# Optimization experiments

Hardware: AMD Instinct MI355X
Metric: run time of the kernel (lower is better)

Reference implementation:

```python
import jax, jax.numpy as jnp
import numpy as np

NEG_SLOPE = 0.2  # LeakyReLU slope used by GAT attention
EPS = 1e-16


def gat_conv(x, edge_index, W, a_src, a_dst, b):
    """One GATConv layer with 'mean' head aggregation.
    x: [N, Fin], edge_index: [2, E] (row 0 = src/j, row 1 = dst/i),
    W: [Fin, H*F], a_src/a_dst: [H, F], b: [F].
    Returns [N, F].
    """
    N = x.shape[0]
    H, F = a_src.shape
    h = (x @ W).reshape(N, H, F)                      # [N, H, F]
    src, dst = edge_index[0], edge_index[1]
    # per-node attention halves, gathered per edge
    as_ = jnp.einsum('nhf,hf->nh', h, a_src)          # [N, H]
    ad_ = jnp.einsum('nhf,hf->nh', h, a_dst)          # [N, H]
    e = jax.nn.leaky_relu(as_[src] + ad_[dst], NEG_SLOPE)  # [E, H]
    # segment softmax over incoming edges of each dst node
    m = jax.ops.segment_max(e, dst, num_segments=N)   # [N, H]
    ex = jnp.exp(e - m[dst])                          # [E, H]
    denom = jax.ops.segment_sum(ex, dst, num_segments=N)
    alpha = ex / (denom[dst] + EPS)                   # [E, H]
    # weighted scatter-aggregate of source features
    out = jax.ops.segment_sum(alpha[:, :, None] * h[src], dst, num_segments=N)  # [N, H, F]
    return out.mean(axis=1) + b                       # mean over heads


def setup_inputs() -> dict:
    key = jax.random.key(0)
    ks = jax.random.split(key, 10)
    N, E = 100000, 1000000
    in_dim, hid, out_dim, H = 128, 32, 16, 4
    x = jax.random.normal(ks[0], (N, in_dim), dtype=jnp.float32)
    edge_index = jax.random.randint(ks[1], (2, E), 0, N, dtype=jnp.int64)
    s1 = 1.0 / np.sqrt(in_dim)
    s2 = 1.0 / np.sqrt(hid)
    W1 = jax.random.uniform(ks[2], (in_dim, H * hid), jnp.float32, -s1, s1)
    a1_src = jax.random.uniform(ks[3], (H, hid), jnp.float32, -s2, s2)
    a1_dst = jax.random.uniform(ks[4], (H, hid), jnp.float32, -s2, s2)
    b1 = jnp.zeros((hid,), jnp.float32)
    s3 = 1.0 / np.sqrt(out_dim)
    W2 = jax.random.uniform(ks[5], (hid, H * out_dim), jnp.float32, -s2, s2)
    a2_src = jax.random.uniform(ks[6], (H, out_dim), jnp.float32, -s3, s3)
    a2_dst = jax.random.uniform(ks[7], (H, out_dim), jnp.float32, -s3, s3)
    b2 = jnp.zeros((out_dim,), jnp.float32)
    return {"x": x, "edge_index": edge_index,
            "W1": W1, "a1_src": a1_src, "a1_dst": a1_dst, "b1": b1,
            "W2": W2, "a2_src": a2_src, "a2_dst": a2_dst, "b2": b2}


def reference(x, edge_index, W1, a1_src, a1_dst, b1, W2, a2_src, a2_dst, b2):
    h = gat_conv(x, edge_index, W1, a1_src, a1_dst, b1)
    h = jax.nn.relu(h)
    # dropout is identity in eval mode
    out = gat_conv(h, edge_index, W2, a2_src, a2_dst, b2)
    return out
```

## Files before the change

kernel.cpp:

```cpp
#include <hip/hip_runtime.h>
#include <math.h>

#define NEG_SLOPE 0.2f
#define EPS_GAT 1e-16f
#define LOG2E 1.4426950408889634f
typedef unsigned int u32;
typedef unsigned short u16;
typedef __attribute__((ext_vector_type(8))) short short8;
typedef __attribute__((ext_vector_type(4))) float f32x4;

__device__ inline u16 f2bf(float x) {
    union { float f; u32 u; } v; v.f = x;
    u32 r = v.u + 0x7FFFu + ((v.u >> 16) & 1u);
    return (u16)(r >> 16);
}
__device__ inline float bf_lo(u32 u) {
    union { u32 i; float f; } v; v.i = u << 16; return v.f;
}
__device__ inline float bf_hi(u32 u) {
    union { u32 i; float f; } v; v.i = u & 0xFFFF0000u; return v.f;
}
__device__ inline float bf1(u16 s) {
    union { u32 i; float f; } v; v.i = ((u32)s) << 16; return v.f;
}
__device__ inline float fast_exp2(float x) {
#if __has_builtin(__builtin_amdgcn_exp2f)
    return __builtin_amdgcn_exp2f(x);
#else
    return exp2f(x);
#endif
}
__device__ inline float lrelu_exp2(float t) {
    return fast_exp2(fmaxf(t, NEG_SLOPE * t));
}


__global__ void degree_prep_kernel(const int* __restrict__ dst, int E,
                                   int* __restrict__ counts, int* __restrict__ rank,
                                   const float* __restrict__ W1,
                                   u16* __restrict__ w1t_hi, u16* __restrict__ w1t_lo,
                                   const float* __restrict__ W2, const float* __restrict__ a2s,
                                   const float* __restrict__ a2d, float* __restrict__ w_as,
                                   float* __restrict__ w_ad, int degBlocks) {
    int b = blockIdx.x;
    if (b < degBlocks) {
        int e = b * 256 + threadIdx.x;
        if (e < E) rank[e] = atomicAdd(&counts[dst[e]], 1);
    } else if (b < degBlocks + 64) {
        int i = (b - degBlocks) * 256 + threadIdx.x;
        int k = i >> 7, n = i & 127;
        float w = W1[i];
        u16 hi = f2bf(w);
        u16 lo = f2bf(w - bf1(hi));
        w1t_hi[n * 128 + k] = hi;
        w1t_lo[n * 128 + k] = lo;
    } else {
        int t = threadIdx.x;
        if (t < 128) {
            int h = t >> 5, k = t & 31;
            float s1 = 0.f, s2 = 0.f;
#pragma unroll
            for (int f = 0; f < 16; ++f) {
                float w = W2[k * 64 + h * 16 + f];
                s1 += w * a2s[h * 16 + f];
                s2 += w * a2d[h * 16 + f];
            }
            w_as[h * 32 + k] = s1;
            w_ad[h * 32 + k] = s2;
        }
    }
}

__global__ __launch_bounds__(1024) void scan_block_kernel(const int* __restrict__ counts, int N,
                                                          int* __restrict__ scanned, int* __restrict__ bsums) {
    __shared__ int tmp[1024];
    int i = blockIdx.x * 1024 + threadIdx.x;
    int v = (i < N) ? counts[i] : 0;
    tmp[threadIdx.x] = v;
    __syncthreads();
    for (int d = 1; d < 1024; d <<= 1) {
        int t = (threadIdx.x >= d) ? tmp[threadIdx.x - d] : 0;
        __syncthreads();
        tmp[threadIdx.x] += t;
        __syncthreads();
    }
    if (i < N) scanned[i] = tmp[threadIdx.x];
    if (threadIdx.x == 1023) bsums[blockIdx.x] = tmp[1023];
}

__global__ __launch_bounds__(256) void scan_partials_kernel(int* __restrict__ bsums, int nb) {
    __shared__ int tmp[256];
    int tid = threadIdx.x;
    int v = (tid < nb) ? bsums[tid] : 0;
    tmp[tid] = v;
    __syncthreads();
    for (int d = 1; d < 256; d <<= 1) {
        int t = (tid >= d) ? tmp[tid - d] : 0;
        __syncthreads();
        tmp[tid] += t;
        __syncthreads();
    }
    if (tid < nb) bsums[tid] = tmp[tid] - v;
}

__global__ void finalize_offsets_kernel(const int* __restrict__ scanned,
                                        const int* __restrict__ bsums_excl, int N,
                                        int* __restrict__ row_off) {
    int i = blockIdx.x * blockDim.x + threadIdx.x;
    if (i < N) {
        int incl = scanned[i] + bsums_excl[i >> 10];
        row_off[i + 1] = incl;
        if (i == 0) row_off[0] = 0;
    }
}

__global__ void fill_csr_kernel(const int* __restrict__ src, const int* __restrict__ dst, int E,
                                const int* __restrict__ row_off, const int* __restrict__ rank,
                                int* __restrict__ csr_src) {
    int e = blockIdx.x * blockDim.x + threadIdx.x;
    if (e < E) {
        int pos = row_off[dst[e]] + rank[e];
        csr_src[pos] = src[e];
    }
}


__global__ __launch_bounds__(256) void gemm1_mfma_kernel(const float* __restrict__ X,
                                                         const u16* __restrict__ w1t_hi,
                                                         const u16* __restrict__ w1t_lo,
                                                         const float* __restrict__ a_src,
                                                         const float* __restrict__ a_dst,
                                                         u16* __restrict__ Hb,
                                                         float* __restrict__ as_,
                                                         float* __restrict__ ad_, int N) {
    __shared__ u16 xsh_hi[64][40];
    __shared__ u16 xsh_lo[64][40];
    __shared__ u16 wbuf[10240];
    __shared__ float ash[128], adsh[128];
    u16* wsh_hi = wbuf;
    u16* wsh_lo = wbuf + 5120;
    int tid = threadIdx.x;
    int wave = tid >> 6, lane = tid & 63, quad = lane >> 4;
    int m0 = blockIdx.x * 64;

    if (tid < 128) { ash[tid] = a_src[tid]; adsh[tid] = a_dst[tid]; }

    f32x4 acc[4][2];
#pragma unroll
    for (int rt = 0; rt < 4; ++rt)
#pragma unroll
        for (int ct = 0; ct < 2; ++ct) acc[rt][ct] = (f32x4)(0.f);

    int xrow = tid >> 2, xkq = (tid & 3) * 8;

    for (int k0 = 0; k0 < 128; k0 += 32) {
        {
            int gr = m0 + xrow;
            float f[8];
            *(float4*)&f[0] = (gr < N) ? *(const float4*)(X + (size_t)gr * 128 + k0 + xkq)
                                       : make_float4(0.f, 0.f, 0.f, 0.f);
            *(float4*)&f[4] = (gr < N) ? *(const float4*)(X + (size_t)gr * 128 + k0 + xkq + 4)
                                       : make_float4(0.f, 0.f, 0.f, 0.f);
            u16 hi[8], lo[8];
#pragma unroll
            for (int i = 0; i < 8; ++i) {
                hi[i] = f2bf(f[i]);
                lo[i] = f2bf(f[i] - bf1(hi[i]));
            }
            *(uint4*)&xsh_hi[xrow][xkq] = *(uint4*)hi;
            *(uint4*)&xsh_lo[xrow][xkq] = *(uint4*)lo;
        }
        {
#pragma unroll
            for (int i = 0; i < 2; ++i) {
                int id = tid * 2 + i;
                int n = id >> 2, part = id & 3;
                *(uint4*)&wsh_hi[n * 40 + part * 8] =
                    ((const uint4*)(w1t_hi + n * 128 + k0))[part];
                *(uint4*)&wsh_lo[n * 40 + part * 8] =
                    ((const uint4*)(w1t_lo + n * 128 + k0))[part];
            }
        }
        __syncthreads();

        short8 bhi[2], blo[2];
#pragma unroll
        for (int ct = 0; ct < 2; ++ct) {
            int n = wave * 32 + ct * 16 + (lane & 15);
            bhi[ct] = *(const short8*)&wsh_hi[n * 40 + quad * 8];
            blo[ct] = *(const short8*)&wsh_lo[n * 40 + quad * 8];
        }
#pragma unroll
        for (int rt = 0; rt < 4; ++rt) {
            int m = rt * 16 + (lane & 15);
            short8 ahi = *(const short8*)&xsh_hi[m][quad * 8];
            short8 alo = *(const short8*)&xsh_lo[m][quad * 8];
#pragma unroll
            for (int ct = 0; ct < 2; ++ct) {
                acc[rt][ct] = __builtin_amdgcn_mfma_f32_16x16x32_bf16(ahi, bhi[ct], acc[rt][ct], 0, 0, 0);
                acc[rt][ct] = __builtin_amdgcn_mfma_f32_16x16x32_bf16(alo, bhi[ct], acc[rt][ct], 0, 0, 0);
                acc[rt][ct] = __builtin_amdgcn_mfma_f32_16x16x32_bf16(ahi, blo[ct], acc[rt][ct], 0, 0, 0);
            }
        }
        __syncthreads();
    }

    const int HS = 130;
#pragma unroll
    for (int rt = 0; rt < 4; ++rt)
#pragma unroll
        for (int ct = 0; ct < 2; ++ct) {
            int col = wave * 32 + ct * 16 + (lane & 15);
#pragma unroll
            for (int r = 0; r < 4; ++r) {
                int row = rt * 16 + quad * 4 + r;
                u16 hv = f2bf(acc[rt][ct][r]);
                int gr = m0 + row;
                if (gr < N) Hb[(size_t)gr * 128 + col] = hv;
                wbuf[row * HS + col] = hv;
            }
        }
    __syncthreads();

    {
        int row = tid >> 2, h = tid & 3;
        int gr = m0 + row;
        if (gr < N) {
            const u32* hr = (const u32*)&wbuf[row * HS + h * 32];
            float s1 = 0.f, s2 = 0.f;
#pragma unroll
            for (int q = 0; q < 16; ++q) {
                u32 u = hr[q];
                float flo = bf_lo(u), fhi = bf_hi(u);
                s1 += flo * ash[h * 32 + 2 * q] + fhi * ash[h * 32 + 2 * q + 1];
                s2 += flo * adsh[h * 32 + 2 * q] + fhi * adsh[h * 32 + 2 * q + 1];
            }
            as_[(size_t)gr * 4 + h] = s1 * LOG2E;
            ad_[(size_t)gr * 4 + h] = s2 * LOG2E;
        }
    }
}


__global__ __launch_bounds__(256) void node_agg128_kernel(const u32* __restrict__ Hb,
                                                          const float* __restrict__ as_,
                                                          const float* __restrict__ ad_,
                                                          const int* __restrict__ row_off,
                                                          const int* __restrict__ csr_src,
                                                          const float* __restrict__ bias,
                                                          const float* __restrict__ w_as,
                                                          const float* __restrict__ w_ad,
                                                          u32* __restrict__ O1,
                                                          float* __restrict__ as2,
                                                          float* __restrict__ ad2, int N) {
    int lane = threadIdx.x & 63;
    int node = __builtin_amdgcn_readfirstlane(blockIdx.x * 4 + (threadIdx.x >> 6));
    if (node >= N) return;
    int start = __builtin_amdgcn_readfirstlane(row_off[node]);
    int end   = __builtin_amdgcn_readfirstlane(row_off[node + 1]);
    int deg = end - start;
    int h = lane >> 4;
    float adh = ad_[node * 4 + h];

    int clamp = (deg > 0) ? deg - 1 : 0;
    int vidx = csr_src[start + min(lane, clamp)];
    int m = min(deg, 64);

    float2 acc = make_float2(0.f, 0.f);
    float den = 0.f;
    int j = 0;
    for (; j + 4 <= m; j += 4) {
        int s0 = __builtin_amdgcn_readlane(vidx, j);
        int s1 = __builtin_amdgcn_readlane(vidx, j + 1);
        int s2 = __builtin_amdgcn_readlane(vidx, j + 2);
        int s3 = __builtin_amdgcn_readlane(vidx, j + 3);
        float a0 = as_[s0 * 4 + h], a1 = as_[s1 * 4 + h];
        float a2 = as_[s2 * 4 + h], a3 = as_[s3 * 4 + h];
        u32 u0 = Hb[s0 * 64 + lane];
        u32 u1 = Hb[s1 * 64 + lane];
        u32 u2 = Hb[s2 * 64 + lane];
        u32 u3 = Hb[s3 * 64 + lane];
        float e0 = lrelu_exp2(a0 + adh), e1 = lrelu_exp2(a1 + adh);
        float e2 = lrelu_exp2(a2 + adh), e3 = lrelu_exp2(a3 + adh);
        acc.x = fmaf(e0, bf_lo(u0), acc.x); acc.y = fmaf(e0, bf_hi(u0), acc.y); den += e0;
        acc.x = fmaf(e1, bf_lo(u1), acc.x); acc.y = fmaf(e1, bf_hi(u1), acc.y); den += e1;
        acc.x = fmaf(e2, bf_lo(u2), acc.x); acc.y = fmaf(e2, bf_hi(u2), acc.y); den += e2;
        acc.x = fmaf(e3, bf_lo(u3), acc.x); acc.y = fmaf(e3, bf_hi(u3), acc.y); den += e3;
    }
    for (; j < m; ++j) {
        int s = __builtin_amdgcn_readlane(vidx, j);
        float e = lrelu_exp2(as_[s * 4 + h] + adh);
        u32 u = Hb[s * 64 + lane];
        acc.x = fmaf(e, bf_lo(u), acc.x); acc.y = fmaf(e, bf_hi(u), acc.y); den += e;
    }
    for (int jj = start + 64; jj < end; ++jj) {
        int s = __builtin_amdgcn_readfirstlane(csr_src[jj]);
        float e = lrelu_exp2(as_[s * 4 + h] + adh);
        u32 u = Hb[s * 64 + lane];
        acc.x = fmaf(e, bf_lo(u), acc.x); acc.y = fmaf(e, bf_hi(u), acc.y); den += e;
    }
    float inv = 1.f / (den + EPS_GAT);
    float px = acc.x * inv, py = acc.y * inv;
    px += __shfl_xor(px, 16); py += __shfl_xor(py, 16);
    px += __shfl_xor(px, 32); py += __shfl_xor(py, 32);

    int f2 = (lane & 15) * 2;
    float2 bv = *(const float2*)&bias[f2];
    float ox = fmaxf(px * 0.25f + bv.x, 0.f);
    float oy = fmaxf(py * 0.25f + bv.y, 0.f);
    if (lane < 16)
        O1[node * 16 + lane] = (u32)f2bf(ox) | ((u32)f2bf(oy) << 16);

    int h2 = lane >> 4;
    float2 wa = *(const float2*)&w_as[h2 * 32 + f2];
    float2 wd = *(const float2*)&w_ad[h2 * 32 + f2];
    float ta = ox * wa.x + oy * wa.y;
    float td = ox * wd.x + oy * wd.y;
    ta += __shfl_xor(ta, 1); td += __shfl_xor(td, 1);
    ta += __shfl_xor(ta, 2); td += __shfl_xor(td, 2);
    ta += __shfl_xor(ta, 4); td += __shfl_xor(td, 4);
    ta += __shfl_xor(ta, 8); td += __shfl_xor(td, 8);
    if ((lane & 15) == 0) {
        as2[node * 4 + h2] = ta * LOG2E;
        ad2[node * 4 + h2] = td * LOG2E;
    }
}


__global__ __launch_bounds__(256) void node_agg32_fused_kernel(const u32* __restrict__ O1,
                                                               const float* __restrict__ as_,
                                                               const float* __restrict__ ad_,
                                                               const int* __restrict__ row_off,
                                                               const int* __restrict__ csr_src,
                                                               const float* __restrict__ W2,
                                                               const float* __restrict__ b2,
                                                               float* __restrict__ Out, int N) {
    __shared__ float w2sh[2048];
    __shared__ float aggsh[4][136];
    int tid = threadIdx.x;
    {
        float4 v = ((const float4*)W2)[tid];
        *(float4*)&w2sh[tid * 4] = v;
        float4 v2 = ((const float4*)W2)[tid + 256];
        *(float4*)&w2sh[(tid + 256) * 4] = v2;
    }

    int lane = tid & 63;
    int nb = tid >> 6;
    int node = __builtin_amdgcn_readfirstlane(blockIdx.x * 4 + nb);
    bool active = node < N;
    int h = lane >> 4, f = lane & 15;
    if (active) {
        int start = __builtin_amdgcn_readfirstlane(row_off[node]);
        int end   = __builtin_amdgcn_readfirstlane(row_off[node + 1]);
        int deg = end - start;
        float adh = ad_[node * 4 + h];

        int clamp = (deg > 0) ? deg - 1 : 0;
        int vidx = csr_src[start + min(lane, clamp)];
        int m = min(deg, 64);

        float2 acc = make_float2(0.f, 0.f);
        float den = 0.f;
        int j = 0;
        for (; j + 4 <= m; j += 4) {
            int s0 = __builtin_amdgcn_readlane(vidx, j);
            int s1 = __builtin_amdgcn_readlane(vidx, j + 1);
            int s2 = __builtin_amdgcn_readlane(vidx, j + 2);
            int s3 = __builtin_amdgcn_readlane(vidx, j + 3);
            float a0 = as_[s0 * 4 + h], a1 = as_[s1 * 4 + h];
            float a2 = as_[s2 * 4 + h], a3 = as_[s3 * 4 + h];
            u32 u0 = O1[s0 * 16 + f];
            u32 u1 = O1[s1 * 16 + f];
            u32 u2 = O1[s2 * 16 + f];
            u32 u3 = O1[s3 * 16 + f];
            float e0 = lrelu_exp2(a0 + adh), e1 = lrelu_exp2(a1 + adh);
            float e2 = lrelu_exp2(a2 + adh), e3 = lrelu_exp2(a3 + adh);
            acc.x = fmaf(e0, bf_lo(u0), acc.x); acc.y = fmaf(e0, bf_hi(u0), acc.y); den += e0;
            acc.x = fmaf(e1, bf_lo(u1), acc.x); acc.y = fmaf(e1, bf_hi(u1), acc.y); den += e1;
            acc.x = fmaf(e2, bf_lo(u2), acc.x); acc.y = fmaf(e2, bf_hi(u2), acc.y); den += e2;
            acc.x = fmaf(e3, bf_lo(u3), acc.x); acc.y = fmaf(e3, bf_hi(u3), acc.y); den += e3;
        }
        for (; j < m; ++j) {
            int s = __builtin_amdgcn_readlane(vidx, j);
            float e = lrelu_exp2(as_[s * 4 + h] + adh);
            u32 u = O1[s * 16 + f];
            acc.x = fmaf(e, bf_lo(u), acc.x); acc.y = fmaf(e, bf_hi(u), acc.y); den += e;
        }
        for (int jj = start + 64; jj < end; ++jj) {
            int s = __builtin_amdgcn_readfirstlane(csr_src[jj]);
            float e = lrelu_exp2(as_[s * 4 + h] + adh);
            u32 u = O1[s * 16 + f];
            acc.x = fmaf(e, bf_lo(u), acc.x); acc.y = fmaf(e, bf_hi(u), acc.y); den += e;
        }
        float inv = 1.f / (den + EPS_GAT);
        aggsh[nb][h * 34 + f * 2]     = acc.x * inv;
        aggsh[nb][h * 34 + f * 2 + 1] = acc.y * inv;
    }
    __syncthreads();

    if (active) {
        int q = h, o = f;
        float s = 0.f;
#pragma unroll
        for (int k = 0; k < 32; ++k)
            s += aggsh[nb][q * 34 + k] * w2sh[k * 64 + q * 16 + o];
        s += __shfl_xor(s, 16);
        s += __shfl_xor(s, 32);
        if (lane < 16)
            Out[(size_t)node * 16 + o] = s * 0.25f + b2[o];
    }
}


extern "C" void kernel_launch(void* const* d_in, const int* in_sizes, int n_in,
                              void* d_out, int out_size, void* d_ws, size_t ws_size,
                              hipStream_t stream) {
    const float* x      = (const float*)d_in[0];
    const int*   eidx   = (const int*)d_in[1];
    const float* W1     = (const float*)d_in[2];
    const float* a1_src = (const float*)d_in[3];
    const float* a1_dst = (const float*)d_in[4];
    const float* b1     = (const float*)d_in[5];
    const float* W2     = (const float*)d_in[6];
    const float* a2_src = (const float*)d_in[7];
    const float* a2_dst = (const float*)d_in[8];
    const float* b2     = (const float*)d_in[9];
    float* out = (float*)d_out;

    const int N = in_sizes[0] / 128;
    const int E = in_sizes[1] / 2;
    const int* src = eidx;
    const int* dst = eidx + E;

    char* base = (char*)d_ws;
    size_t off = 0;
    auto carve = [&](size_t bytes) -> char* {
        off = (off + 255) & ~(size_t)255;
        char* p = base + off;
        off += bytes;
        return p;
    };
    int* counts   = (int*)carve((size_t)N * 4);
    int* scanned  = (int*)carve((size_t)N * 4);
    int* bsums    = (int*)carve(256 * 4);
    int* row_off  = (int*)carve((size_t)(N + 1) * 4);
    int* rank     = (int*)carve((size_t)E * 4);
    int* csr_src  = (int*)carve((size_t)E * 4);
    u16* w1t_hi   = (u16*)carve(128 * 128 * 2);
    u16* w1t_lo   = (u16*)carve(128 * 128 * 2);
    u16* h1b      = (u16*)carve((size_t)N * 128 * 2);
    u32* out1b    = (u32*)carve((size_t)N * 16 * 4);
    float* as1  = (float*)carve((size_t)N * 4 * 4);
    float* ad1  = (float*)carve((size_t)N * 4 * 4);
    float* as2  = (float*)carve((size_t)N * 4 * 4);
    float* ad2  = (float*)carve((size_t)N * 4 * 4);
    float* w_as = (float*)carve(4 * 32 * 4);
    float* w_ad = (float*)carve(4 * 32 * 4);
    (void)ws_size; (void)n_in; (void)out_size;

    hipMemsetAsync(counts, 0, (size_t)N * 4, stream);
    int degBlocks = (E + 255) / 256;
    degree_prep_kernel<<<degBlocks + 65, 256, 0, stream>>>(dst, E, counts, rank,
                                                           W1, w1t_hi, w1t_lo,
                                                           W2, a2_src, a2_dst, w_as, w_ad,
                                                           degBlocks);
    int nb = (N + 1023) / 1024;
    scan_block_kernel<<<nb, 1024, 0, stream>>>(counts, N, scanned, bsums);
    scan_partials_kernel<<<1, 256, 0, stream>>>(bsums, nb);
    finalize_offsets_kernel<<<(N + 255) / 256, 256, 0, stream>>>(scanned, bsums, N, row_off);
    fill_csr_kernel<<<(E + 255) / 256, 256, 0, stream>>>(src, dst, E, row_off, rank, csr_src);

    gemm1_mfma_kernel<<<(N + 63) / 64, 256, 0, stream>>>(x, w1t_hi, w1t_lo, a1_src, a1_dst,
                                                         h1b, as1, ad1, N);
    node_agg128_kernel<<<(N + 3) / 4, 256, 0, stream>>>((const u32*)h1b, as1, ad1,
                                                        row_off, csr_src, b1, w_as, w_ad,
                                                        out1b, as2, ad2, N);

    node_agg32_fused_kernel<<<(N + 3) / 4, 256, 0, stream>>>(out1b, as2, ad2, row_off,
                                                             csr_src, W2, b2, out, N);
}
```

Baseline: 298.5 us.

## Merge CSR build and layer-1 GEMM into one cooperative persistent kernel

Replaces the memset, degree count, three scan kernels, CSR fill and the GEMM1 launch with a single cooperative kernel that separates phases with grid-wide syncs. Within one phase, part of the grid runs the GEMM tiles while the remaining blocks do the degree atomics, so the two overlap. This removes several launch gaps and small-kernel tails, at the cost of grid.sync overhead, a fixed persistent grid size, and fewer blocks per phase.

```diff
diff --git a/kernel.cpp b/kernel.cpp
--- a/kernel.cpp
+++ b/kernel.cpp
@@ -1,5 +1,8 @@
 #include <hip/hip_runtime.h>
+#include <hip/hip_cooperative_groups.h>
 #include <math.h>
+
+namespace cg = cooperative_groups;
 
 #define NEG_SLOPE 0.2f
 #define EPS_GAT 1e-16f
@@ -35,209 +38,222 @@
 }
 
 
-__global__ void degree_prep_kernel(const int* __restrict__ dst, int E,
-                                   int* __restrict__ counts, int* __restrict__ rank,
-                                   const float* __restrict__ W1,
-                                   u16* __restrict__ w1t_hi, u16* __restrict__ w1t_lo,
-                                   const float* __restrict__ W2, const float* __restrict__ a2s,
-                                   const float* __restrict__ a2d, float* __restrict__ w_as,
-                                   float* __restrict__ w_ad, int degBlocks) {
-    int b = blockIdx.x;
-    if (b < degBlocks) {
-        int e = b * 256 + threadIdx.x;
-        if (e < E) rank[e] = atomicAdd(&counts[dst[e]], 1);
-    } else if (b < degBlocks + 64) {
-        int i = (b - degBlocks) * 256 + threadIdx.x;
+struct CoopArgs {
+    const int* src; const int* dst; int E; int N;
+    int* counts; int* rank;
+    const float* X; const float* W1;
+    const float* a1_src; const float* a1_dst;
+    const float* W2; const float* a2s; const float* a2d;
+    float* w_as; float* w_ad;
+    u16* w1t_hi; u16* w1t_lo;
+    u16* Hb; float* as1; float* ad1;
+    int* scanned; int* bsums; int* row_off; int* csr_src;
+    int gemmBlocks;
+};
+
+__global__ __launch_bounds__(256) void coop_kernel(CoopArgs A) {
+    cg::grid_group grid = cg::this_grid();
+    __shared__ __align__(16) u16 xsh_hi[64 * 40];
+    __shared__ __align__(16) u16 xsh_lo[64 * 40];
+    __shared__ __align__(16) u16 wbuf[10240];
+    __shared__ float ash[128], adsh[128];
+    int* stmp = (int*)xsh_hi;
+
+    int tid = threadIdx.x, bid = blockIdx.x;
+    int nB = gridDim.x;
+    int gtid = bid * 256 + tid, gstride = nB * 256;
+
+    for (int i = gtid; i < A.N; i += gstride) A.counts[i] = 0;
+    for (int i = gtid; i < 16384; i += gstride) {
         int k = i >> 7, n = i & 127;
-        float w = W1[i];
+        float w = A.W1[i];
         u16 hi = f2bf(w);
         u16 lo = f2bf(w - bf1(hi));
-        w1t_hi[n * 128 + k] = hi;
-        w1t_lo[n * 128 + k] = lo;
+        A.w1t_hi[n * 128 + k] = hi;
+        A.w1t_lo[n * 128 + k] = lo;
+    }
+    if (gtid < 128) {
+        int h = gtid >> 5, k = gtid & 31;
+        float s1 = 0.f, s2 = 0.f;
+#pragma unroll
+        for (int f = 0; f < 16; ++f) {
+            float w = A.W2[k * 64 + h * 16 + f];
+            s1 += w * A.a2s[h * 16 + f];
+            s2 += w * A.a2d[h * 16 + f];
+        }
+        A.w_as[h * 32 + k] = s1;
+        A.w_ad[h * 32 + k] = s2;
+    }
+    grid.sync();
+
+    if (bid < A.gemmBlocks) {
+        if (tid < 128) { ash[tid] = A.a1_src[tid]; adsh[tid] = A.a1_dst[tid]; }
+        u16* wsh_hi = wbuf;
+        u16* wsh_lo = wbuf + 5120;
+        int wave = tid >> 6, lane = tid & 63, quad = lane >> 4;
+        int xrow = tid >> 2, xkq = (tid & 3) * 8;
+        int tiles = (A.N + 63) >> 6;
+        for (int t = bid; t < tiles; t += A.gemmBlocks) {
+            __syncthreads();
+            int m0 = t * 64;
+            f32x4 acc[4][2];
+#pragma unroll
+            for (int rt = 0; rt < 4; ++rt)
+#pragma unroll
+                for (int ct = 0; ct < 2; ++ct) acc[rt][ct] = (f32x4)(0.f);
+
+            for (int k0 = 0; k0 < 128; k0 += 32) {
+                {
+                    int gr = m0 + xrow;
+                    float f[8];
+                    *(float4*)&f[0] = (gr < A.N) ? *(const float4*)(A.X + (size_t)gr * 128 + k0 + xkq)
+                                                 : make_float4(0.f, 0.f, 0.f, 0.f);
+                    *(float4*)&f[4] = (gr < A.N) ? *(const float4*)(A.X + (size_t)gr * 128 + k0 + xkq + 4)
+                                                 : make_float4(0.f, 0.f, 0.f, 0.f);
+                    u16 hi[8], lo[8];
+#pragma unroll
+                    for (int i = 0; i < 8; ++i) {
+                        hi[i] = f2bf(f[i]);
+                        lo[i] = f2bf(f[i] - bf1(hi[i]));
+                    }
+                    *(uint4*)&xsh_hi[xrow * 40 + xkq] = *(uint4*)hi;
+                    *(uint4*)&xsh_lo[xrow * 40 + xkq] = *(uint4*)lo;
+                }
+                {
+#pragma unroll
+                    for (int i = 0; i < 2; ++i) {
+                        int id = tid * 2 + i;
+                        int n = id >> 2, part = id & 3;
+                        *(uint4*)&wsh_hi[n * 40 + part * 8] =
+                            ((const uint4*)(A.w1t_hi + n * 128 + k0))[part];
+                        *(uint4*)&wsh_lo[n * 40 + part * 8] =
+                            ((const uint4*)(A.w1t_lo + n * 128 + k0))[part];
+                    }
+                }
+                __syncthreads();
+
+                short8 bhi[2], blo[2];
+#pragma unroll
+                for (int ct = 0; ct < 2; ++ct) {
+                    int n = wave * 32 + ct * 16 + (lane & 15);
+                    bhi[ct] = *(const short8*)&wsh_hi[n * 40 + quad * 8];
+                    blo[ct] = *(const short8*)&wsh_lo[n * 40 + quad * 8];
+                }
+#pragma unroll
+                for (int rt = 0; rt < 4; ++rt) {
+                    int m = rt * 16 + (lane & 15);
+                    short8 ahi = *(const short8*)&xsh_hi[m * 40 + quad * 8];
+                    short8 alo = *(const short8*)&xsh_lo[m * 40 + quad * 8];
+#pragma unroll
+                    for (int ct = 0; ct < 2; ++ct) {
+                        acc[rt][ct] = __builtin_amdgcn_mfma_f32_16x16x32_bf16(ahi, bhi[ct], acc[rt][ct], 0, 0, 0);
+                        acc[rt][ct] = __builtin_amdgcn_mfma_f32_16x16x32_bf16(alo, bhi[ct], acc[rt][ct], 0, 0, 0);
+                        acc[rt][ct] = __builtin_amdgcn_mfma_f32_16x16x32_bf16(ahi, blo[ct], acc[rt][ct], 0, 0, 0);
+                    }
+                }
+                __syncthreads();
+            }
+
+            const int HS = 130;
+#pragma unroll
+            for (int rt = 0; rt < 4; ++rt)
+#pragma unroll
+                for (int ct = 0; ct < 2; ++ct) {
+                    int col = wave * 32 + ct * 16 + (lane & 15);
+#pragma unroll
+                    for (int r = 0; r < 4; ++r) {
+                        int row = rt * 16 + quad * 4 + r;
+                        u16 hv = f2bf(acc[rt][ct][r]);
+                        int gr = m0 + row;
+                        if (gr < A.N) A.Hb[(size_t)gr * 128 + col] = hv;
+                        wbuf[row * HS + col] = hv;
+                    }
+                }
+            __syncthreads();
+
+            {
+                int row = tid >> 2, h = tid & 3;
+                int gr = m0 + row;
+                if (gr < A.N) {
+                    const u32* hr = (const u32*)&wbuf[row * HS + h * 32];
+                    float s1 = 0.f, s2 = 0.f;
+#pragma unroll
+                    for (int q = 0; q < 16; ++q) {
+                        u32 u = hr[q];
+                        float flo = bf_lo(u), fhi = bf_hi(u);
+                        s1 += flo * ash[h * 32 + 2 * q] + fhi * ash[h * 32 + 2 * q + 1];
+                        s2 += flo * adsh[h * 32 + 2 * q] + fhi * adsh[h * 32 + 2 * q + 1];
+                    }
+                    A.as1[(size_t)gr * 4 + h] = s1 * LOG2E;
+                    A.ad1[(size_t)gr * 4 + h] = s2 * LOG2E;
+                }
+            }
+        }
     } else {
-        int t = threadIdx.x;
-        if (t < 128) {
-            int h = t >> 5, k = t & 31;
-            float s1 = 0.f, s2 = 0.f;
-#pragma unroll
-            for (int f = 0; f < 16; ++f) {
-                float w = W2[k * 64 + h * 16 + f];
-                s1 += w * a2s[h * 16 + f];
-                s2 += w * a2d[h * 16 + f];
+        int nd = nB - A.gemmBlocks;
+        for (int e = (bid - A.gemmBlocks) * 256 + tid; e < A.E; e += nd * 256)
+            A.rank[e] = atomicAdd(&A.counts[A.dst[e]], 1);
+    }
+    grid.sync();
+
+    {
+        int chunks = (A.N + 1023) >> 10;
+        for (int c = bid; c < chunks; c += nB) {
+            int idx = (c << 10) + tid * 4;
+            int4 v = make_int4(0, 0, 0, 0);
+            if (idx + 3 < A.N) v = *(const int4*)(A.counts + idx);
+            else {
+                if (idx < A.N)     v.x = A.counts[idx];
+                if (idx + 1 < A.N) v.y = A.counts[idx + 1];
+                if (idx + 2 < A.N) v.z = A.counts[idx + 2];
             }
-            w_as[h * 32 + k] = s1;
-            w_ad[h * 32 + k] = s2;
-        }
-    }
-}
-
-__global__ __launch_bounds__(1024) void scan_block_kernel(const int* __restrict__ counts, int N,
-                                                          int* __restrict__ scanned, int* __restrict__ bsums) {
-    __shared__ int tmp[1024];
-    int i = blockIdx.x * 1024 + threadIdx.x;
-    int v = (i < N) ? counts[i] : 0;
-    tmp[threadIdx.x] = v;
-    __syncthreads();
-    for (int d = 1; d < 1024; d <<= 1) {
-        int t = (threadIdx.x >= d) ? tmp[threadIdx.x - d] : 0;
+            int p0 = v.x, p1 = p0 + v.y, p2 = p1 + v.z, p3 = p2 + v.w;
+            __syncthreads();
+            stmp[tid] = p3;
+            __syncthreads();
+            for (int d = 1; d < 256; d <<= 1) {
+                int t_ = (tid >= d) ? stmp[tid - d] : 0;
+                __syncthreads();
+                stmp[tid] += t_;
+                __syncthreads();
+            }
+            int excl = stmp[tid] - p3;
+            if (idx + 3 < A.N) {
+                int4 o = make_int4(excl + p0, excl + p1, excl + p2, excl + p3);
+                *(int4*)(A.scanned + idx) = o;
+            } else {
+                if (idx < A.N)     A.scanned[idx]     = excl + p0;
+                if (idx + 1 < A.N) A.scanned[idx + 1] = excl + p1;
+                if (idx + 2 < A.N) A.scanned[idx + 2] = excl + p2;
+            }
+            if (tid == 255) A.bsums[c] = stmp[255];
+        }
+    }
+    grid.sync();
+
+    if (bid == 0) {
+        int chunks = (A.N + 1023) >> 10;
+        int v = (tid < chunks) ? A.bsums[tid] : 0;
+        stmp[tid] = v;
         __syncthreads();
-        tmp[threadIdx.x] += t;
-        __syncthreads();
-    }
-    if (i < N) scanned[i] = tmp[threadIdx.x];
-    if (threadIdx.x == 1023) bsums[blockIdx.x] = tmp[1023];
-}
-
-__global__ __launch_bounds__(256) void scan_partials_kernel(int* __restrict__ bsums, int nb) {
-    __shared__ int tmp[256];
-    int tid = threadIdx.x;
-    int v = (tid < nb) ? bsums[tid] : 0;
-    tmp[tid] = v;
-    __syncthreads();
-    for (int d = 1; d < 256; d <<= 1) {
-        int t = (tid >= d) ? tmp[tid - d] : 0;
-        __syncthreads();
-        tmp[tid] += t;
-        __syncthreads();
-    }
-    if (tid < nb) bsums[tid] = tmp[tid] - v;
-}
-
-__global__ void finalize_offsets_kernel(const int* __restrict__ scanned,
-                                        const int* __restrict__ bsums_excl, int N,
-                                        int* __restrict__ row_off) {
-    int i = blockIdx.x * blockDim.x + threadIdx.x;
-    if (i < N) {
-        int incl = scanned[i] + bsums_excl[i >> 10];
-        row_off[i + 1] = incl;
-        if (i == 0) row_off[0] = 0;
-    }
-}
-
-__global__ void fill_csr_kernel(const int* __restrict__ src, const int* __restrict__ dst, int E,
-                                const int* __restrict__ row_off, const int* __restrict__ rank,
-                                int* __restrict__ csr_src) {
-    int e = blockIdx.x * blockDim.x + threadIdx.x;
-    if (e < E) {
-        int pos = row_off[dst[e]] + rank[e];
-        csr_src[pos] = src[e];
-    }
-}
-
-
-__global__ __launch_bounds__(256) void gemm1_mfma_kernel(const float* __restrict__ X,
-                                                         const u16* __restrict__ w1t_hi,
-                                                         const u16* __restrict__ w1t_lo,
-                                                         const float* __restrict__ a_src,
-                                                         const float* __restrict__ a_dst,
-                                                         u16* __restrict__ Hb,
-                                                         float* __restrict__ as_,
-                                                         float* __restrict__ ad_, int N) {
-    __shared__ u16 xsh_hi[64][40];
-    __shared__ u16 xsh_lo[64][40];
-    __shared__ u16 wbuf[10240];
-    __shared__ float ash[128], adsh[128];
-    u16* wsh_hi = wbuf;
-    u16* wsh_lo = wbuf + 5120;
-    int tid = threadIdx.x;
-    int wave = tid >> 6, lane = tid & 63, quad = lane >> 4;
-    int m0 = blockIdx.x * 64;
-
-    if (tid < 128) { ash[tid] = a_src[tid]; adsh[tid] = a_dst[tid]; }
-
-    f32x4 acc[4][2];
-#pragma unroll
-    for (int rt = 0; rt < 4; ++rt)
-#pragma unroll
-        for (int ct = 0; ct < 2; ++ct) acc[rt][ct] = (f32x4)(0.f);
-
-    int xrow = tid >> 2, xkq = (tid & 3) * 8;
-
-    for (int k0 = 0; k0 < 128; k0 += 32) {
-        {
-            int gr = m0 + xrow;
-            float f[8];
-            *(float4*)&f[0] = (gr < N) ? *(const float4*)(X + (size_t)gr * 128 + k0 + xkq)
-                                       : make_float4(0.f, 0.f, 0.f, 0.f);
-            *(float4*)&f[4] = (gr < N) ? *(const float4*)(X + (size_t)gr * 128 + k0 + xkq + 4)
-                                       : make_float4(0.f, 0.f, 0.f, 0.f);
-            u16 hi[8], lo[8];
-#pragma unroll
-            for (int i = 0; i < 8; ++i) {
-                hi[i] = f2bf(f[i]);
-                lo[i] = f2bf(f[i] - bf1(hi[i]));
-            }
-            *(uint4*)&xsh_hi[xrow][xkq] = *(uint4*)hi;
-            *(uint4*)&xsh_lo[xrow][xkq] = *(uint4*)lo;
-        }
-        {
-#pragma unroll
-            for (int i = 0; i < 2; ++i) {
-                int id = tid * 2 + i;
-                int n = id >> 2, part = id & 3;
-                *(uint4*)&wsh_hi[n * 40 + part * 8] =
-                    ((const uint4*)(w1t_hi + n * 128 + k0))[part];
-                *(uint4*)&wsh_lo[n * 40 + part * 8] =
-                    ((const uint4*)(w1t_lo + n * 128 + k0))[part];
-            }
-        }
-        __syncthreads();
-
-        short8 bhi[2], blo[2];
-#pragma unroll
-        for (int ct = 0; ct < 2; ++ct) {
-            int n = wave * 32 + ct * 16 + (lane & 15);
-            bhi[ct] = *(const short8*)&wsh_hi[n * 40 + quad * 8];
-            blo[ct] = *(const short8*)&wsh_lo[n * 40 + quad * 8];
-        }
-#pragma unroll
-        for (int rt = 0; rt < 4; ++rt) {
-            int m = rt * 16 + (lane & 15);
-            short8 ahi = *(const short8*)&xsh_hi[m][quad * 8];
-            short8 alo = *(const short8*)&xsh_lo[m][quad * 8];
-#pragma unroll
-            for (int ct = 0; ct < 2; ++ct) {
-                acc[rt][ct] = __builtin_amdgcn_mfma_f32_16x16x32_bf16(ahi, bhi[ct], acc[rt][ct], 0, 0, 0);
-                acc[rt][ct] = __builtin_amdgcn_mfma_f32_16x16x32_bf16(alo, bhi[ct], acc[rt][ct], 0, 0, 0);
-                acc[rt][ct] = __builtin_amdgcn_mfma_f32_16x16x32_bf16(ahi, blo[ct], acc[rt][ct], 0, 0, 0);
-            }
-        }
-        __syncthreads();
-    }
-
-    const int HS = 130;
-#pragma unroll
-    for (int rt = 0; rt < 4; ++rt)
-#pragma unroll
-        for (int ct = 0; ct < 2; ++ct) {
-            int col = wave * 32 + ct * 16 + (lane & 15);
-#pragma unroll
-            for (int r = 0; r < 4; ++r) {
-                int row = rt * 16 + quad * 4 + r;
-                u16 hv = f2bf(acc[rt][ct][r]);
-                int gr = m0 + row;
-                if (gr < N) Hb[(size_t)gr * 128 + col] = hv;
-                wbuf[row * HS + col] = hv;
-            }
-        }
-    __syncthreads();
-
-    {
-        int row = tid >> 2, h = tid & 3;
-        int gr = m0 + row;
-        if (gr < N) {
-            const u32* hr = (const u32*)&wbuf[row * HS + h * 32];
-            float s1 = 0.f, s2 = 0.f;
-#pragma unroll
-            for (int q = 0; q < 16; ++q) {
-                u32 u = hr[q];
-                float flo = bf_lo(u), fhi = bf_hi(u);
-                s1 += flo * ash[h * 32 + 2 * q] + fhi * ash[h * 32 + 2 * q + 1];
-                s2 += flo * adsh[h * 32 + 2 * q] + fhi * adsh[h * 32 + 2 * q + 1];
-            }
-            as_[(size_t)gr * 4 + h] = s1 * LOG2E;
-            ad_[(size_t)gr * 4 + h] = s2 * LOG2E;
-        }
+        for (int d = 1; d < 256; d <<= 1) {
+            int t_ = (tid >= d) ? stmp[tid - d] : 0;
+            __syncthreads();
+            stmp[tid] += t_;
+            __syncthreads();
+        }
+        if (tid < chunks) A.bsums[tid] = stmp[tid] - v;
+    }
+    grid.sync();
+
+    for (int i = gtid; i < A.N; i += gstride)
+        A.row_off[i + 1] = A.scanned[i] + A.bsums[i >> 10];
+    if (gtid == 0) A.row_off[0] = 0;
+    grid.sync();
+
+    for (int e = gtid; e < A.E; e += gstride) {
+        int pos = A.row_off[A.dst[e]] + A.rank[e];
+        A.csr_src[pos] = A.src[e];
     }
 }
 
@@ -459,24 +475,34 @@
     float* w_ad = (float*)carve(4 * 32 * 4);
     (void)ws_size; (void)n_in; (void)out_size;
 
-    hipMemsetAsync(counts, 0, (size_t)N * 4, stream);
-    int degBlocks = (E + 255) / 256;
-    degree_prep_kernel<<<degBlocks + 65, 256, 0, stream>>>(dst, E, counts, rank,
-                                                           W1, w1t_hi, w1t_lo,
-                                                           W2, a2_src, a2_dst, w_as, w_ad,
-                                                           degBlocks);
-    int nb = (N + 1023) / 1024;
-    scan_block_kernel<<<nb, 1024, 0, stream>>>(counts, N, scanned, bsums);
-    scan_partials_kernel<<<1, 256, 0, stream>>>(bsums, nb);
-    finalize_offsets_kernel<<<(N + 255) / 256, 256, 0, stream>>>(scanned, bsums, N, row_off);
-    fill_csr_kernel<<<(E + 255) / 256, 256, 0, stream>>>(src, dst, E, row_off, rank, csr_src);
-
-    gemm1_mfma_kernel<<<(N + 63) / 64, 256, 0, stream>>>(x, w1t_hi, w1t_lo, a1_src, a1_dst,
-                                                         h1b, as1, ad1, N);
+    int blocksPerCU = 2;
+    if (hipOccupancyMaxActiveBlocksPerMultiprocessor(&blocksPerCU, coop_kernel, 256, 0) != hipSuccess)
+        blocksPerCU = 2;
+    if (blocksPerCU < 1) blocksPerCU = 1;
+    if (blocksPerCU > 4) blocksPerCU = 4;
+    int grid = 256 * blocksPerCU;
+
+    CoopArgs A;
+    A.src = src; A.dst = dst; A.E = E; A.N = N;
+    A.counts = counts; A.rank = rank;
+    A.X = x; A.W1 = W1;
+    A.a1_src = a1_src; A.a1_dst = a1_dst;
+    A.W2 = W2; A.a2s = a2_src; A.a2d = a2_dst;
+    A.w_as = w_as; A.w_ad = w_ad;
+    A.w1t_hi = w1t_hi; A.w1t_lo = w1t_lo;
+    A.Hb = h1b; A.as1 = as1; A.ad1 = ad1;
+    A.scanned = scanned; A.bsums = bsums; A.row_off = row_off; A.csr_src = csr_src;
+    A.gemmBlocks = (grid * 3) / 5;
+    if (A.gemmBlocks < 1) A.gemmBlocks = 1;
+    if (A.gemmBlocks > grid - 1) A.gemmBlocks = grid - 1;
+
+    void* params[] = { &A };
+    hipLaunchCooperativeKernel((const void*)coop_kernel, dim3(grid), dim3(256),
+                               params, 0, stream);
+
     node_agg128_kernel<<<(N + 3) / 4, 256, 0, stream>>>((const u32*)h1b, as1, ad1,
                                                         row_off, csr_src, b1, w_as, w_ad,
                                                         out1b, as2, ad2, N);
-
     node_agg32_fused_kernel<<<(N + 3) / 4, 256, 0, stream>>>(out1b, as2, ad2, row_off,
                                                              csr_src, W2, b2, out, N);
 }
```

Result: slower. 480.7 us (+61.1%).

## Fuse CSR build kernels with last-block scan and grid-stride degree counting

Applied to the files above, without the earlier changes.

Merges the two-level prefix scan into one kernel, where the last block to finish (tracked by an atomic counter) scans the partial sums. Offset finalization and the CSR fill are combined into one kernel, and the degree counting now runs as a fixed 2048-block grid-stride loop. The goal is fewer kernel launches and less serialization in graph preprocessing. Aggregation kernels also get occupancy hints via launch bounds. It adds a memset for the done counter and relies on threadfence ordering for the last-block scan.

```diff
diff --git a/kernel.cpp b/kernel.cpp
--- a/kernel.cpp
+++ b/kernel.cpp
@@ -35,29 +35,26 @@
 }
 
 
-__global__ void degree_prep_kernel(const int* __restrict__ dst, int E,
-                                   int* __restrict__ counts, int* __restrict__ rank,
-                                   const float* __restrict__ W1,
+__global__ void prep_degree_kernel(const float* __restrict__ W1,
                                    u16* __restrict__ w1t_hi, u16* __restrict__ w1t_lo,
                                    const float* __restrict__ W2, const float* __restrict__ a2s,
                                    const float* __restrict__ a2d, float* __restrict__ w_as,
-                                   float* __restrict__ w_ad, int degBlocks) {
+                                   float* __restrict__ w_ad,
+                                   const int* __restrict__ dst, int E,
+                                   int* __restrict__ counts, int* __restrict__ rank) {
     int b = blockIdx.x;
-    if (b < degBlocks) {
-        int e = b * 256 + threadIdx.x;
-        if (e < E) rank[e] = atomicAdd(&counts[dst[e]], 1);
-    } else if (b < degBlocks + 64) {
-        int i = (b - degBlocks) * 256 + threadIdx.x;
+    int tid = threadIdx.x;
+    if (b < 64) {
+        int i = b * 256 + tid;
         int k = i >> 7, n = i & 127;
         float w = W1[i];
         u16 hi = f2bf(w);
         u16 lo = f2bf(w - bf1(hi));
         w1t_hi[n * 128 + k] = hi;
         w1t_lo[n * 128 + k] = lo;
-    } else {
-        int t = threadIdx.x;
-        if (t < 128) {
-            int h = t >> 5, k = t & 31;
+    } else if (b == 64) {
+        if (tid < 128) {
+            int h = tid >> 5, k = tid & 31;
             float s1 = 0.f, s2 = 0.f;
 #pragma unroll
             for (int f = 0; f < 16; ++f) {
@@ -68,59 +65,10 @@
             w_as[h * 32 + k] = s1;
             w_ad[h * 32 + k] = s2;
         }
-    }
-}
-
-__global__ __launch_bounds__(1024) void scan_block_kernel(const int* __restrict__ counts, int N,
-                                                          int* __restrict__ scanned, int* __restrict__ bsums) {
-    __shared__ int tmp[1024];
-    int i = blockIdx.x * 1024 + threadIdx.x;
-    int v = (i < N) ? counts[i] : 0;
-    tmp[threadIdx.x] = v;
-    __syncthreads();
-    for (int d = 1; d < 1024; d <<= 1) {
-        int t = (threadIdx.x >= d) ? tmp[threadIdx.x - d] : 0;
-        __syncthreads();
-        tmp[threadIdx.x] += t;
-        __syncthreads();
-    }
-    if (i < N) scanned[i] = tmp[threadIdx.x];
-    if (threadIdx.x == 1023) bsums[blockIdx.x] = tmp[1023];
-}
-
-__global__ __launch_bounds__(256) void scan_partials_kernel(int* __restrict__ bsums, int nb) {
-    __shared__ int tmp[256];
-    int tid = threadIdx.x;
-    int v = (tid < nb) ? bsums[tid] : 0;
-    tmp[tid] = v;
-    __syncthreads();
-    for (int d = 1; d < 256; d <<= 1) {
-        int t = (tid >= d) ? tmp[tid - d] : 0;
-        __syncthreads();
-        tmp[tid] += t;
-        __syncthreads();
-    }
-    if (tid < nb) bsums[tid] = tmp[tid] - v;
-}
-
-__global__ void finalize_offsets_kernel(const int* __restrict__ scanned,
-                                        const int* __restrict__ bsums_excl, int N,
-                                        int* __restrict__ row_off) {
-    int i = blockIdx.x * blockDim.x + threadIdx.x;
-    if (i < N) {
-        int incl = scanned[i] + bsums_excl[i >> 10];
-        row_off[i + 1] = incl;
-        if (i == 0) row_off[0] = 0;
-    }
-}
-
-__global__ void fill_csr_kernel(const int* __restrict__ src, const int* __restrict__ dst, int E,
-                                const int* __restrict__ row_off, const int* __restrict__ rank,
-                                int* __restrict__ csr_src) {
-    int e = blockIdx.x * blockDim.x + threadIdx.x;
-    if (e < E) {
-        int pos = row_off[dst[e]] + rank[e];
-        csr_src[pos] = src[e];
+    } else {
+        int nd = gridDim.x - 65;
+        for (int e = (b - 65) * 256 + tid; e < E; e += nd * 256)
+            rank[e] = atomicAdd(&counts[dst[e]], 1);
     }
 }
 
@@ -133,25 +81,24 @@
                                                          u16* __restrict__ Hb,
                                                          float* __restrict__ as_,
                                                          float* __restrict__ ad_, int N) {
-    __shared__ u16 xsh_hi[64][40];
-    __shared__ u16 xsh_lo[64][40];
-    __shared__ u16 wbuf[10240];
+    __shared__ __align__(16) u16 xsh_hi[64 * 40];
+    __shared__ __align__(16) u16 xsh_lo[64 * 40];
+    __shared__ __align__(16) u16 wbuf[10240];
     __shared__ float ash[128], adsh[128];
-    u16* wsh_hi = wbuf;
-    u16* wsh_lo = wbuf + 5120;
     int tid = threadIdx.x;
     int wave = tid >> 6, lane = tid & 63, quad = lane >> 4;
     int m0 = blockIdx.x * 64;
 
     if (tid < 128) { ash[tid] = a_src[tid]; adsh[tid] = a_dst[tid]; }
+    u16* wsh_hi = wbuf;
+    u16* wsh_lo = wbuf + 5120;
+    int xrow = tid >> 2, xkq = (tid & 3) * 8;
 
     f32x4 acc[4][2];
 #pragma unroll
     for (int rt = 0; rt < 4; ++rt)
 #pragma unroll
         for (int ct = 0; ct < 2; ++ct) acc[rt][ct] = (f32x4)(0.f);
-
-    int xrow = tid >> 2, xkq = (tid & 3) * 8;
 
     for (int k0 = 0; k0 < 128; k0 += 32) {
         {
@@ -167,8 +114,8 @@
                 hi[i] = f2bf(f[i]);
                 lo[i] = f2bf(f[i] - bf1(hi[i]));
             }
-            *(uint4*)&xsh_hi[xrow][xkq] = *(uint4*)hi;
-            *(uint4*)&xsh_lo[xrow][xkq] = *(uint4*)lo;
+            *(uint4*)&xsh_hi[xrow * 40 + xkq] = *(uint4*)hi;
+            *(uint4*)&xsh_lo[xrow * 40 + xkq] = *(uint4*)lo;
         }
         {
 #pragma unroll
@@ -193,8 +140,8 @@
 #pragma unroll
         for (int rt = 0; rt < 4; ++rt) {
             int m = rt * 16 + (lane & 15);
-            short8 ahi = *(const short8*)&xsh_hi[m][quad * 8];
-            short8 alo = *(const short8*)&xsh_lo[m][quad * 8];
+            short8 ahi = *(const short8*)&xsh_hi[m * 40 + quad * 8];
+            short8 alo = *(const short8*)&xsh_lo[m * 40 + quad * 8];
 #pragma unroll
             for (int ct = 0; ct < 2; ++ct) {
                 acc[rt][ct] = __builtin_amdgcn_mfma_f32_16x16x32_bf16(ahi, bhi[ct], acc[rt][ct], 0, 0, 0);
@@ -242,17 +189,75 @@
 }
 
 
-__global__ __launch_bounds__(256) void node_agg128_kernel(const u32* __restrict__ Hb,
-                                                          const float* __restrict__ as_,
-                                                          const float* __restrict__ ad_,
-                                                          const int* __restrict__ row_off,
-                                                          const int* __restrict__ csr_src,
-                                                          const float* __restrict__ bias,
-                                                          const float* __restrict__ w_as,
-                                                          const float* __restrict__ w_ad,
-                                                          u32* __restrict__ O1,
-                                                          float* __restrict__ as2,
-                                                          float* __restrict__ ad2, int N) {
+__global__ __launch_bounds__(1024) void scan_kernel(const int* __restrict__ counts, int N,
+                                                    int* __restrict__ scanned,
+                                                    int* __restrict__ bsums,
+                                                    int* __restrict__ done, int nchunks) {
+    __shared__ int tmp[1024];
+    __shared__ int flag;
+    int tid = threadIdx.x;
+    int i = (blockIdx.x << 10) + tid;
+    int v = (i < N) ? counts[i] : 0;
+    tmp[tid] = v;
+    __syncthreads();
+    for (int d = 1; d < 1024; d <<= 1) {
+        int t = (tid >= d) ? tmp[tid - d] : 0;
+        __syncthreads();
+        tmp[tid] += t;
+        __syncthreads();
+    }
+    if (i < N) scanned[i] = tmp[tid];
+    if (tid == 1023) bsums[blockIdx.x] = tmp[1023];
+    __syncthreads();
+    if (tid == 0) {
+        __threadfence();
+        int prev = atomicAdd(done, 1);
+        flag = (prev == (int)gridDim.x - 1);
+    }
+    __syncthreads();
+    if (flag) {
+        __threadfence();
+        int vv = (tid < nchunks) ? bsums[tid] : 0;
+        tmp[tid] = vv;
+        __syncthreads();
+        for (int d = 1; d < 1024; d <<= 1) {
+            int t = (tid >= d) ? tmp[tid - d] : 0;
+            __syncthreads();
+            tmp[tid] += t;
+            __syncthreads();
+        }
+        if (tid < nchunks) bsums[tid] = tmp[tid] - vv;
+    }
+}
+
+
+__global__ void fill_finalize_kernel(const int* __restrict__ src, const int* __restrict__ dst,
+                                     int E, int N, const int* __restrict__ counts,
+                                     const int* __restrict__ scanned, const int* __restrict__ bsums,
+                                     const int* __restrict__ rank, int* __restrict__ row_off,
+                                     int* __restrict__ csr_src) {
+    int t = blockIdx.x * blockDim.x + threadIdx.x;
+    if (t <= N)
+        row_off[t] = (t == 0) ? 0 : scanned[t - 1] + bsums[(t - 1) >> 10];
+    if (t < E) {
+        int d = dst[t];
+        int startd = scanned[d] + bsums[d >> 10] - counts[d];
+        csr_src[startd + rank[t]] = src[t];
+    }
+}
+
+
+__global__ __launch_bounds__(256, 8) void node_agg128_kernel(const u32* __restrict__ Hb,
+                                                             const float* __restrict__ as_,
+                                                             const float* __restrict__ ad_,
+                                                             const int* __restrict__ row_off,
+                                                             const int* __restrict__ csr_src,
+                                                             const float* __restrict__ bias,
+                                                             const float* __restrict__ w_as,
+                                                             const float* __restrict__ w_ad,
+                                                             u32* __restrict__ O1,
+                                                             float* __restrict__ as2,
+                                                             float* __restrict__ ad2, int N) {
     int lane = threadIdx.x & 63;
     int node = __builtin_amdgcn_readfirstlane(blockIdx.x * 4 + (threadIdx.x >> 6));
     if (node >= N) return;
@@ -327,14 +332,14 @@
 }
 
 
-__global__ __launch_bounds__(256) void node_agg32_fused_kernel(const u32* __restrict__ O1,
-                                                               const float* __restrict__ as_,
-                                                               const float* __restrict__ ad_,
-                                                               const int* __restrict__ row_off,
-                                                               const int* __restrict__ csr_src,
-                                                               const float* __restrict__ W2,
-                                                               const float* __restrict__ b2,
-                                                               float* __restrict__ Out, int N) {
+__global__ __launch_bounds__(256, 8) void node_agg32_fused_kernel(const u32* __restrict__ O1,
+                                                                  const float* __restrict__ as_,
+                                                                  const float* __restrict__ ad_,
+                                                                  const int* __restrict__ row_off,
+                                                                  const int* __restrict__ csr_src,
+                                                                  const float* __restrict__ W2,
+                                                                  const float* __restrict__ b2,
+                                                                  float* __restrict__ Out, int N) {
     __shared__ float w2sh[2048];
     __shared__ float aggsh[4][136];
     int tid = threadIdx.x;
@@ -443,10 +448,11 @@
     };
     int* counts   = (int*)carve((size_t)N * 4);
     int* scanned  = (int*)carve((size_t)N * 4);
-    int* bsums    = (int*)carve(256 * 4);
+    int* bsums    = (int*)carve(1024 * 4);
+    int* done     = (int*)carve(256);
     int* row_off  = (int*)carve((size_t)(N + 1) * 4);
     int* rank     = (int*)carve((size_t)E * 4);
-    int* csr_src  = (int*)carve((size_t)E * 4);
+    int* csr_src  = (int*)carve(((size_t)E + 64) * 4);
     u16* w1t_hi   = (u16*)carve(128 * 128 * 2);
     u16* w1t_lo   = (u16*)carve(128 * 128 * 2);
     u16* h1b      = (u16*)carve((size_t)N * 128 * 2);
@@ -460,19 +466,25 @@
     (void)ws_size; (void)n_in; (void)out_size;
 
     hipMemsetAsync(counts, 0, (size_t)N * 4, stream);
-    int degBlocks = (E + 255) / 256;
-    degree_prep_kernel<<<degBlocks + 65, 256, 0, stream>>>(dst, E, counts, rank,
-                                                           W1, w1t_hi, w1t_lo,
-                                                           W2, a2_src, a2_dst, w_as, w_ad,
-                                                           degBlocks);
-    int nb = (N + 1023) / 1024;
-    scan_block_kernel<<<nb, 1024, 0, stream>>>(counts, N, scanned, bsums);
-    scan_partials_kernel<<<1, 256, 0, stream>>>(bsums, nb);
-    finalize_offsets_kernel<<<(N + 255) / 256, 256, 0, stream>>>(scanned, bsums, N, row_off);
-    fill_csr_kernel<<<(E + 255) / 256, 256, 0, stream>>>(src, dst, E, row_off, rank, csr_src);
+    hipMemsetAsync(done, 0, 4, stream);
+
+    prep_degree_kernel<<<65 + 2048, 256, 0, stream>>>(W1, w1t_hi, w1t_lo,
+                                                      W2, a2_src, a2_dst, w_as, w_ad,
+                                                      dst, E, counts, rank);
 
     gemm1_mfma_kernel<<<(N + 63) / 64, 256, 0, stream>>>(x, w1t_hi, w1t_lo, a1_src, a1_dst,
                                                          h1b, as1, ad1, N);
+
+    int nchunks = (N + 1023) / 1024;
+    scan_kernel<<<nchunks, 1024, 0, stream>>>(counts, N, scanned, bsums, done, nchunks);
+
+    {
+        int total = (E > N + 1) ? E : (N + 1);
+        fill_finalize_kernel<<<(total + 255) / 256, 256, 0, stream>>>(src, dst, E, N, counts,
+                                                                      scanned, bsums, rank,
+                                                                      row_off, csr_src);
+    }
+
     node_agg128_kernel<<<(N + 3) / 4, 256, 0, stream>>>((const u32*)h1b, as1, ad1,
                                                         row_off, csr_src, b1, w_as, w_ad,
                                                         out1b, as2, ad2, N);
```

Result: slower. 319.0 us (+6.9%).
